# Performance work log

Hardware: AMD Instinct MI355X
Metric: run time of the kernel (lower is better)

The kernel has to match this reference:

```python
import jax, jax.numpy as jnp
import numpy as np

N_NODES = 100000
N_EDGES = 1600000
NFEAT, NHID, NCLASS = 128, 64, 16


def gcn_conv(x, W, edge_index, edge_weight, num_nodes):
    # PyG GCNConv (normalize=False, add_self_loops=False, bias=False):
    # h = x @ W ; out[i] = sum over edges (j->i) of edge_weight * h[j]
    h = x @ W                                  # [N, out]
    src, dst = edge_index[0], edge_index[1]
    msgs = h[src] * edge_weight[:, None]       # [E, out] gathered messages
    return jax.ops.segment_sum(msgs, dst, num_segments=num_nodes)


def setup_inputs() -> dict:
    key = jax.random.key(0)
    k = jax.random.split(key, 7)
    x = jax.random.normal(k[0], (N_NODES, NFEAT), dtype=jnp.float32)
    edge_index1 = jax.random.randint(k[1], (2, N_EDGES), 0, N_NODES, dtype=jnp.int32)
    edge_index2 = jax.random.randint(k[2], (2, N_EDGES), 0, N_NODES, dtype=jnp.int32)
    edge_weight1 = jax.random.uniform(k[3], (N_EDGES,), dtype=jnp.float32)
    edge_weight2 = jax.random.uniform(k[4], (N_EDGES,), dtype=jnp.float32)
    # Glorot-style linear weights (GCNConv lin, bias=False)
    W1 = jax.random.normal(k[5], (NFEAT, NHID), dtype=jnp.float32) / np.sqrt(NFEAT)
    W2 = jax.random.normal(k[6], (NHID, NCLASS), dtype=jnp.float32) / np.sqrt(NHID)
    return {"x": x, "edge_index1": edge_index1, "edge_index2": edge_index2,
            "edge_weight1": edge_weight1, "edge_weight2": edge_weight2,
            "W1": W1, "W2": W2}


def reference(x, edge_index1, edge_index2, edge_weight1, edge_weight2, W1, W2):
    n = x.shape[0]
    h = jax.nn.relu(gcn_conv(x, W1, edge_index1, edge_weight1, n))
    out = gcn_conv(h, W2, edge_index2, edge_weight2, n)
    return out
```

## Files before the change

kernel.cpp:

```cpp
#include <hip/hip_runtime.h>
#include <hip/hip_bf16.h>


#define EPB 4096
#define NBMAX 512
#define CAP 6144

__global__ __launch_bounds__(256) void gemm1_hist_kernel(
        const float* __restrict__ x, const float* __restrict__ W1,
        __hip_bfloat16* __restrict__ h1,
        const int* __restrict__ ei1, const int* __restrict__ ei2,
        int* __restrict__ hist_g, int n_nodes, int n_edges, int nblk, int nb,
        int gemm_blocks) {
    __shared__ float As[32][132];
    __shared__ float Bs[32][64];
    __shared__ int hist[NBMAX];
    int tid = threadIdx.x;

    if (blockIdx.x < gemm_blocks) {
        int node0 = blockIdx.x * 128;
        int n4 = (tid & 31) * 4;
        int f8 = (tid >> 5) * 8;
        float acc[4][8];
#pragma unroll
        for (int i = 0; i < 4; ++i)
#pragma unroll
            for (int j = 0; j < 8; ++j) acc[i][j] = 0.f;

        const float4* x4 = reinterpret_cast<const float4*>(x);
        const float4* W4 = reinterpret_cast<const float4*>(W1);

        for (int s = 0; s < 4; ++s) {
#pragma unroll
            for (int j = 0; j < 4; ++j) {
                int idx = tid + j * 256;
                int n = idx >> 3;
                int kq = idx & 7;
                float4 v = make_float4(0.f, 0.f, 0.f, 0.f);
                if (node0 + n < n_nodes) v = x4[(size_t)(node0 + n) * 32 + s * 8 + kq];
                int k4 = kq * 4;
                As[k4 + 0][n] = v.x;
                As[k4 + 1][n] = v.y;
                As[k4 + 2][n] = v.z;
                As[k4 + 3][n] = v.w;
            }
#pragma unroll
            for (int j = 0; j < 2; ++j) {
                int idx = tid + j * 256;
                int k = idx >> 4;
                int fq = idx & 15;
                *reinterpret_cast<float4*>(&Bs[k][fq * 4]) = W4[(size_t)(s * 32 + k) * 16 + fq];
            }
            __syncthreads();
#pragma unroll
            for (int kk = 0; kk < 32; ++kk) {
                float4 a = *reinterpret_cast<const float4*>(&As[kk][n4]);
                float4 b0 = *reinterpret_cast<const float4*>(&Bs[kk][f8]);
                float4 b1 = *reinterpret_cast<const float4*>(&Bs[kk][f8 + 4]);
                float av[4] = {a.x, a.y, a.z, a.w};
                float bv[8] = {b0.x, b0.y, b0.z, b0.w, b1.x, b1.y, b1.z, b1.w};
#pragma unroll
                for (int i = 0; i < 4; ++i)
#pragma unroll
                    for (int j = 0; j < 8; ++j) acc[i][j] += av[i] * bv[j];
            }
            __syncthreads();
        }
#pragma unroll
        for (int i = 0; i < 4; ++i) {
            int n = node0 + n4 + i;
            if (n < n_nodes) {
                __hip_bfloat16 tmp[8];
#pragma unroll
                for (int j = 0; j < 8; ++j) tmp[j] = __float2bfloat16(acc[i][j]);
                *reinterpret_cast<uint4*>(&h1[(size_t)n * 64 + f8]) =
                    *reinterpret_cast<const uint4*>(tmp);
            }
        }
    } else {
        int blk = blockIdx.x - gemm_blocks;
        int layer = (blk >= nblk) ? 1 : 0;
        int lblk = blk - layer * nblk;
        const int* ei = layer ? ei2 : ei1;
        for (int i = tid; i < nb; i += 256) hist[i] = 0;
        __syncthreads();
        int e0 = lblk * EPB;
#pragma unroll
        for (int j = 0; j < EPB / 256; ++j) {
            int e = e0 + tid + j * 256;
            if (e < n_edges) atomicAdd(&hist[ei[n_edges + e] >> 8], 1);
        }
        __syncthreads();
        int base = layer * nb * nblk;
        for (int i = tid; i < nb; i += 256) hist_g[base + i * nblk + lblk] = hist[i];
    }
}

__global__ void scan_local_k(int* __restrict__ data, int* __restrict__ bsums, int n) {
    __shared__ int tmp[1024];
    int i = blockIdx.x * 1024 + threadIdx.x;
    int v = (i < n) ? data[i] : 0;
    tmp[threadIdx.x] = v;
    __syncthreads();
    for (int off = 1; off < 1024; off <<= 1) {
        int t = (threadIdx.x >= off) ? tmp[threadIdx.x - off] : 0;
        __syncthreads();
        tmp[threadIdx.x] += t;
        __syncthreads();
    }
    if (i < n) data[i] = tmp[threadIdx.x] - v;
    if (threadIdx.x == 1023) bsums[blockIdx.x] = tmp[1023];
}

__global__ void bin_scatter_kernel(const int* __restrict__ ei1, const int* __restrict__ ei2,
                                   const float* __restrict__ ew1, const float* __restrict__ ew2,
                                   const int* __restrict__ scan_g, const int* __restrict__ bsums,
                                   int2* __restrict__ rec_out,
                                   int n_edges, int nblk, int nb, int nbk) {
    __shared__ int2 srec[EPB];
    __shared__ unsigned short sbkt[EPB];
    __shared__ int loff[NBMAX], cur[NBMAX], gbase[NBMAX];
    __shared__ int p[256];
    __shared__ int bscan[512];
    int tid = threadIdx.x, blk = blockIdx.x;
    int layer = (blk >= nblk) ? 1 : 0;
    int lblk = blk - layer * nblk;
    const int* ei = layer ? ei2 : ei1;
    const float* ew = layer ? ew2 : ew1;
    int n_scan_tot = 2 * nb * nblk;
    int total = 2 * n_edges;
    int base = layer * nb * nblk;
    int e0 = lblk * EPB;
    int cnt = min(EPB, n_edges - e0);

    {
        int t2 = tid * 2;
        int v0 = (t2 < nbk) ? bsums[t2] : 0;
        int v1 = (t2 + 1 < nbk) ? bsums[t2 + 1] : 0;
        p[tid] = v0 + v1;
        __syncthreads();
        for (int off = 1; off < 256; off <<= 1) {
            int t = (tid >= off) ? p[tid - off] : 0;
            __syncthreads();
            p[tid] += t;
            __syncthreads();
        }
        int pb = (tid > 0) ? p[tid - 1] : 0;
        bscan[t2] = pb;
        bscan[t2 + 1] = pb + v0;
        __syncthreads();
    }

    for (int i = tid; i < nb; i += 256) {
        int l = base + i * nblk + lblk;
        int g = scan_g[l] + bscan[l >> 10];
        int nxt = (l + 1 < n_scan_tot) ? (scan_g[l + 1] + bscan[(l + 1) >> 10]) : total;
        gbase[i] = g;
        loff[i] = nxt - g;
    }
    __syncthreads();
    int b0 = tid * 2;
    int c0 = (b0 < nb) ? loff[b0] : 0;
    int c1 = (b0 + 1 < nb) ? loff[b0 + 1] : 0;
    p[tid] = c0 + c1;
    __syncthreads();
    for (int off = 1; off < 256; off <<= 1) {
        int t = (tid >= off) ? p[tid - off] : 0;
        __syncthreads();
        p[tid] += t;
        __syncthreads();
    }
    int pbase = (tid > 0) ? p[tid - 1] : 0;
    __syncthreads();
    if (b0 < nb)     { loff[b0] = pbase;          cur[b0] = pbase; }
    if (b0 + 1 < nb) { loff[b0 + 1] = pbase + c0; cur[b0 + 1] = pbase + c0; }
    __syncthreads();
#pragma unroll
    for (int j = 0; j < EPB / 256; ++j) {
        int e = e0 + tid + j * 256;
        if (e < n_edges) {
            int s = ei[e], d = ei[n_edges + e];
            int b = d >> 8;
            int r = atomicAdd(&cur[b], 1);
            srec[r] = make_int2(s | ((d & 255) << 20), __float_as_int(ew[e]));
            sbkt[r] = (unsigned short)b;
        }
    }
    __syncthreads();
    for (int i = tid; i < cnt; i += 256) {
        int b = sbkt[i];
        rec_out[gbase[b] + (i - loff[b])] = srec[i];
    }
}


__global__ __launch_bounds__(256) void bucket_sort_kernel(
        const int2* __restrict__ rec_in, const int* __restrict__ scan_g,
        const int* __restrict__ bsums,
        int2* __restrict__ rec_out, int* __restrict__ rowptr1, int* __restrict__ rowptr2,
        int n_nodes, int n_edges, int nblk, int nb, int nbk) {
    __shared__ int2 srec[CAP];
    __shared__ int hist[256], cur[256], rp[256], p[256];
    __shared__ int bscan[512];
    int tid = threadIdx.x, b = blockIdx.x;
    int layer = (b >= nb) ? 1 : 0;
    int lb = b - layer * nb;
    int* rowptr = layer ? rowptr2 : rowptr1;
    int sh = layer ? 6 : 7;
    int total = 2 * n_edges;

    {
        int t2 = tid * 2;
        int v0 = (t2 < nbk) ? bsums[t2] : 0;
        int v1 = (t2 + 1 < nbk) ? bsums[t2 + 1] : 0;
        p[tid] = v0 + v1;
        __syncthreads();
        for (int off = 1; off < 256; off <<= 1) {
            int t = (tid >= off) ? p[tid - off] : 0;
            __syncthreads();
            p[tid] += t;
            __syncthreads();
        }
        int pb = (tid > 0) ? p[tid - 1] : 0;
        bscan[t2] = pb;
        bscan[t2 + 1] = pb + v0;
        __syncthreads();
    }

    int l0 = b * nblk;
    int start = scan_g[l0] + bscan[l0 >> 10];
    int l1 = (b + 1) * nblk;
    int end = (b + 1 < 2 * nb) ? (scan_g[l1] + bscan[l1 >> 10]) : total;
    int cnt = end - start;
    hist[tid] = 0;
    __syncthreads();
    for (int i = tid; i < cnt; i += 256) {
        int2 r = rec_in[start + i];
        atomicAdd(&hist[(r.x >> 20) & 255], 1);
    }
    __syncthreads();
    int v = hist[tid];
    rp[tid] = v;
    __syncthreads();
    for (int off = 1; off < 256; off <<= 1) {
        int t = (tid >= off) ? rp[tid - off] : 0;
        __syncthreads();
        rp[tid] += t;
        __syncthreads();
    }
    int excl = rp[tid] - v;
    cur[tid] = excl;
    int node = (lb << 8) + tid;
    if (node < n_nodes) rowptr[node] = start + excl;
    if (lb == nb - 1 && tid == 0) rowptr[n_nodes] = end;
    __syncthreads();
    for (int i = tid; i < cnt; i += 256) {
        int2 r = rec_in[start + i];
        int rk = atomicAdd(&cur[(r.x >> 20) & 255], 1);
        r.x = (r.x & 0xFFFFF) << sh;
        if (rk < CAP) srec[rk] = r;
    }
    __syncthreads();
    int lim = min(cnt, CAP);
    for (int i = tid; i < lim; i += 256) rec_out[start + i] = srec[i];
}


#define G1_EDGE(rr, aa) \
    aa += __bfloat162float(*(const __hip_bfloat16*)(h1b + (unsigned)(rr).x + f2)) * \
          __int_as_float((rr).y)

__global__ __launch_bounds__(256) void gather1_kernel(const __hip_bfloat16* __restrict__ h1,
                                                      const int* __restrict__ rowptr,
                                                      const int2* __restrict__ rec,
                                                      const float* __restrict__ W2,
                                                      float* __restrict__ h2, int n_nodes) {
    int tid = threadIdx.x;
    int w = tid >> 6, f = tid & 63;
    unsigned f2 = (unsigned)(f << 1);
    const char* h1b = (const char*)h1;
    int n = blockIdx.x * 4 + w;
    bool valid = (n < n_nodes);
    int i = 0, end = 0;
    if (valid) { i = rowptr[n]; end = rowptr[n + 1]; }
    float a0 = 0.f, a1 = 0.f, a2 = 0.f, a3 = 0.f;
    float a4 = 0.f, a5 = 0.f, a6 = 0.f, a7 = 0.f;
    float a8 = 0.f, a9 = 0.f, a10 = 0.f, a11 = 0.f;
    float a12 = 0.f, a13 = 0.f, a14 = 0.f, a15 = 0.f;
    for (; i + 15 < end; i += 16) {
        int2 r0 = rec[i],      r1 = rec[i + 1],  r2 = rec[i + 2],  r3 = rec[i + 3];
        int2 r4 = rec[i + 4],  r5 = rec[i + 5],  r6 = rec[i + 6],  r7 = rec[i + 7];
        int2 r8 = rec[i + 8],  r9 = rec[i + 9],  r10 = rec[i + 10], r11 = rec[i + 11];
        int2 r12 = rec[i + 12], r13 = rec[i + 13], r14 = rec[i + 14], r15 = rec[i + 15];
        G1_EDGE(r0, a0);   G1_EDGE(r1, a1);   G1_EDGE(r2, a2);   G1_EDGE(r3, a3);
        G1_EDGE(r4, a4);   G1_EDGE(r5, a5);   G1_EDGE(r6, a6);   G1_EDGE(r7, a7);
        G1_EDGE(r8, a8);   G1_EDGE(r9, a9);   G1_EDGE(r10, a10); G1_EDGE(r11, a11);
        G1_EDGE(r12, a12); G1_EDGE(r13, a13); G1_EDGE(r14, a14); G1_EDGE(r15, a15);
    }
    for (; i + 7 < end; i += 8) {
        int2 r0 = rec[i],     r1 = rec[i + 1], r2 = rec[i + 2], r3 = rec[i + 3];
        int2 r4 = rec[i + 4], r5 = rec[i + 5], r6 = rec[i + 6], r7 = rec[i + 7];
        G1_EDGE(r0, a0); G1_EDGE(r1, a1); G1_EDGE(r2, a2); G1_EDGE(r3, a3);
        G1_EDGE(r4, a4); G1_EDGE(r5, a5); G1_EDGE(r6, a6); G1_EDGE(r7, a7);
    }
    for (; i + 3 < end; i += 4) {
        int2 r0 = rec[i], r1 = rec[i + 1], r2 = rec[i + 2], r3 = rec[i + 3];
        G1_EDGE(r0, a0); G1_EDGE(r1, a1); G1_EDGE(r2, a2); G1_EDGE(r3, a3);
    }
    for (; i < end; ++i) {
        int2 r = rec[i];
        G1_EDGE(r, a0);
    }
    float s0 = ((a0 + a1) + (a2 + a3)) + ((a4 + a5) + (a6 + a7));
    float s1 = ((a8 + a9) + (a10 + a11)) + ((a12 + a13) + (a14 + a15));
    float r = fmaxf(s0 + s1, 0.f);
    int c = f & 15, kq = f >> 4;
    float pacc = 0.f;
#pragma unroll
    for (int j = 0; j < 16; ++j) {
        int k = kq * 16 + j;
        float rk = __shfl(r, k, 64);
        pacc += rk * W2[k * 16 + c];
    }
    pacc += __shfl_xor(pacc, 16, 64);
    pacc += __shfl_xor(pacc, 32, 64);
    if (valid && f < 16) h2[(size_t)n * 16 + f] = pacc;
}


#define G2_EDGE(rr, aa) \
    aa += *(const float*)(h2b + (unsigned)(rr).x + f4) * __int_as_float((rr).y)

__global__ void gather2_kernel(const float* __restrict__ h2,
                               const int* __restrict__ rowptr,
                               const int2* __restrict__ rec,
                               float* __restrict__ out, int n_nodes) {
    int n = blockIdx.x * 16 + (threadIdx.x >> 4);
    if (n >= n_nodes) return;
    int f = threadIdx.x & 15;
    unsigned f4 = (unsigned)(f << 2);
    const char* h2b = (const char*)h2;
    int i = rowptr[n], end = rowptr[n + 1];
    float a0 = 0.f, a1 = 0.f, a2 = 0.f, a3 = 0.f;
    float a4 = 0.f, a5 = 0.f, a6 = 0.f, a7 = 0.f;
    for (; i + 7 < end; i += 8) {
        int2 r0 = rec[i],     r1 = rec[i + 1], r2 = rec[i + 2], r3 = rec[i + 3];
        int2 r4 = rec[i + 4], r5 = rec[i + 5], r6 = rec[i + 6], r7 = rec[i + 7];
        G2_EDGE(r0, a0); G2_EDGE(r1, a1); G2_EDGE(r2, a2); G2_EDGE(r3, a3);
        G2_EDGE(r4, a4); G2_EDGE(r5, a5); G2_EDGE(r6, a6); G2_EDGE(r7, a7);
    }
    for (; i + 3 < end; i += 4) {
        int2 r0 = rec[i], r1 = rec[i + 1], r2 = rec[i + 2], r3 = rec[i + 3];
        G2_EDGE(r0, a0); G2_EDGE(r1, a1); G2_EDGE(r2, a2); G2_EDGE(r3, a3);
    }
    for (; i < end; ++i) {
        int2 r = rec[i];
        G2_EDGE(r, a0);
    }
    out[(size_t)n * 16 + f] = (((a0 + a1) + (a2 + a3)) + ((a4 + a5) + (a6 + a7)));
}


extern "C" void kernel_launch(void* const* d_in, const int* in_sizes, int n_in,
                              void* d_out, int out_size, void* d_ws, size_t ws_size,
                              hipStream_t stream) {
    const float* x   = (const float*)d_in[0];
    const int*   ei1 = (const int*)d_in[1];
    const int*   ei2 = (const int*)d_in[2];
    const float* ew1 = (const float*)d_in[3];
    const float* ew2 = (const float*)d_in[4];
    const float* W1  = (const float*)d_in[5];
    const float* W2  = (const float*)d_in[6];

    const int n_nodes = in_sizes[0] / 128;
    const int n_edges = in_sizes[1] / 2;
    const int nb   = (n_nodes + 255) >> 8;
    const int nblk = (n_edges + EPB - 1) / EPB;
    const int n_scan_tot = 2 * nb * nblk;
    const int scan_blocks = (n_scan_tot + 1023) / 1024;
    const int gemm_blocks = (n_nodes + 127) / 128;

    int2* rec2   = (int2*)d_ws;
    int2* recbuf = rec2 + (size_t)2 * n_edges;
    int*  hist_g = (int*)(recbuf + (size_t)2 * n_edges);
    int*  bsums  = hist_g + n_scan_tot;
    int*  rowptr1 = bsums + 512;
    int*  rowptr2 = rowptr1 + n_nodes + 1;
    __hip_bfloat16* h1 = (__hip_bfloat16*)(rowptr2 + n_nodes + 1);
    float* h2 = (float*)recbuf;
    float* out = (float*)d_out;

    gemm1_hist_kernel<<<gemm_blocks + 2 * nblk, 256, 0, stream>>>(
        x, W1, h1, ei1, ei2, hist_g, n_nodes, n_edges, nblk, nb, gemm_blocks);
    scan_local_k<<<scan_blocks, 1024, 0, stream>>>(hist_g, bsums, n_scan_tot);
    bin_scatter_kernel<<<2 * nblk, 256, 0, stream>>>(ei1, ei2, ew1, ew2, hist_g, bsums,
                                                     recbuf, n_edges, nblk, nb, scan_blocks);
    bucket_sort_kernel<<<2 * nb, 256, 0, stream>>>(recbuf, hist_g, bsums, rec2,
                                                   rowptr1, rowptr2,
                                                   n_nodes, n_edges, nblk, nb, scan_blocks);

    gather1_kernel<<<(n_nodes + 3) / 4, 256, 0, stream>>>(h1, rowptr1, rec2, W2, h2, n_nodes);
    gather2_kernel<<<(n_nodes + 15) / 16, 256, 0, stream>>>(h2, rowptr2, rec2, out, n_nodes);
}
```

Before: 300.4 us.

## Split bucket sort per layer and overlap layer-2 sort with layer-1 gather

The single bucket sort kernel is split in two. The layer-1 sort runs alone, and the layer-2 sort now runs in the same launch as the layer-1 gather/GEMM, as extra blocks. The shared-memory staging buffer is also removed, so sorted records are scattered straight to global memory. The aim is to fill the GPU during the small layer-2 sort and cut LDS use so more blocks fit per CU. The cost is less coalesced record writes, and h2 must not overlap the layer-2 source records that are read concurrently.

```diff
diff --git a/kernel.cpp b/kernel.cpp
--- a/kernel.cpp
+++ b/kernel.cpp
@@ -4,7 +4,6 @@
 
 #define EPB 4096
 #define NBMAX 512
-#define CAP 6144
 
 __global__ __launch_bounds__(256) void gemm1_hist_kernel(
         const float* __restrict__ x, const float* __restrict__ W1,
@@ -194,20 +193,14 @@
 }
 
 
-__global__ __launch_bounds__(256) void bucket_sort_kernel(
+__global__ __launch_bounds__(256) void bucket_sort_l1_kernel(
         const int2* __restrict__ rec_in, const int* __restrict__ scan_g,
         const int* __restrict__ bsums,
-        int2* __restrict__ rec_out, int* __restrict__ rowptr1, int* __restrict__ rowptr2,
+        int2* __restrict__ rec_out, int* __restrict__ rowptr1,
         int n_nodes, int n_edges, int nblk, int nb, int nbk) {
-    __shared__ int2 srec[CAP];
     __shared__ int hist[256], cur[256], rp[256], p[256];
     __shared__ int bscan[512];
     int tid = threadIdx.x, b = blockIdx.x;
-    int layer = (b >= nb) ? 1 : 0;
-    int lb = b - layer * nb;
-    int* rowptr = layer ? rowptr2 : rowptr1;
-    int sh = layer ? 6 : 7;
-    int total = 2 * n_edges;
 
     {
         int t2 = tid * 2;
@@ -230,7 +223,7 @@
     int l0 = b * nblk;
     int start = scan_g[l0] + bscan[l0 >> 10];
     int l1 = (b + 1) * nblk;
-    int end = (b + 1 < 2 * nb) ? (scan_g[l1] + bscan[l1 >> 10]) : total;
+    int end = scan_g[l1] + bscan[l1 >> 10];
     int cnt = end - start;
     hist[tid] = 0;
     __syncthreads();
@@ -250,19 +243,16 @@
     }
     int excl = rp[tid] - v;
     cur[tid] = excl;
-    int node = (lb << 8) + tid;
-    if (node < n_nodes) rowptr[node] = start + excl;
-    if (lb == nb - 1 && tid == 0) rowptr[n_nodes] = end;
+    int node = (b << 8) + tid;
+    if (node < n_nodes) rowptr1[node] = start + excl;
+    if (b == nb - 1 && tid == 0) rowptr1[n_nodes] = end;
     __syncthreads();
     for (int i = tid; i < cnt; i += 256) {
         int2 r = rec_in[start + i];
         int rk = atomicAdd(&cur[(r.x >> 20) & 255], 1);
-        r.x = (r.x & 0xFFFFF) << sh;
-        if (rk < CAP) srec[rk] = r;
-    }
-    __syncthreads();
-    int lim = min(cnt, CAP);
-    for (int i = tid; i < lim; i += 256) rec_out[start + i] = srec[i];
+        r.x = (r.x & 0xFFFFF) << 7;
+        rec_out[start + rk] = r;
+    }
 }
 
 
@@ -270,61 +260,125 @@
     aa += __bfloat162float(*(const __hip_bfloat16*)(h1b + (unsigned)(rr).x + f2)) * \
           __int_as_float((rr).y)
 
-__global__ __launch_bounds__(256) void gather1_kernel(const __hip_bfloat16* __restrict__ h1,
-                                                      const int* __restrict__ rowptr,
-                                                      const int2* __restrict__ rec,
-                                                      const float* __restrict__ W2,
-                                                      float* __restrict__ h2, int n_nodes) {
+__global__ __launch_bounds__(256) void sortl2_gather1_kernel(
+        const int2* __restrict__ rec_in, const int* __restrict__ scan_g,
+        const int* __restrict__ bsums, int2* __restrict__ rec2,
+        int* __restrict__ rowptr2,
+        const __hip_bfloat16* __restrict__ h1, const int* __restrict__ rowptr1,
+        const float* __restrict__ W2, float* __restrict__ h2,
+        int n_nodes, int n_edges, int nblk, int nb, int nbk) {
+    __shared__ int hist[256], cur[256], rp[256], p[256];
+    __shared__ int bscan[512];
     int tid = threadIdx.x;
-    int w = tid >> 6, f = tid & 63;
-    unsigned f2 = (unsigned)(f << 1);
-    const char* h1b = (const char*)h1;
-    int n = blockIdx.x * 4 + w;
-    bool valid = (n < n_nodes);
-    int i = 0, end = 0;
-    if (valid) { i = rowptr[n]; end = rowptr[n + 1]; }
-    float a0 = 0.f, a1 = 0.f, a2 = 0.f, a3 = 0.f;
-    float a4 = 0.f, a5 = 0.f, a6 = 0.f, a7 = 0.f;
-    float a8 = 0.f, a9 = 0.f, a10 = 0.f, a11 = 0.f;
-    float a12 = 0.f, a13 = 0.f, a14 = 0.f, a15 = 0.f;
-    for (; i + 15 < end; i += 16) {
-        int2 r0 = rec[i],      r1 = rec[i + 1],  r2 = rec[i + 2],  r3 = rec[i + 3];
-        int2 r4 = rec[i + 4],  r5 = rec[i + 5],  r6 = rec[i + 6],  r7 = rec[i + 7];
-        int2 r8 = rec[i + 8],  r9 = rec[i + 9],  r10 = rec[i + 10], r11 = rec[i + 11];
-        int2 r12 = rec[i + 12], r13 = rec[i + 13], r14 = rec[i + 14], r15 = rec[i + 15];
-        G1_EDGE(r0, a0);   G1_EDGE(r1, a1);   G1_EDGE(r2, a2);   G1_EDGE(r3, a3);
-        G1_EDGE(r4, a4);   G1_EDGE(r5, a5);   G1_EDGE(r6, a6);   G1_EDGE(r7, a7);
-        G1_EDGE(r8, a8);   G1_EDGE(r9, a9);   G1_EDGE(r10, a10); G1_EDGE(r11, a11);
-        G1_EDGE(r12, a12); G1_EDGE(r13, a13); G1_EDGE(r14, a14); G1_EDGE(r15, a15);
-    }
-    for (; i + 7 < end; i += 8) {
-        int2 r0 = rec[i],     r1 = rec[i + 1], r2 = rec[i + 2], r3 = rec[i + 3];
-        int2 r4 = rec[i + 4], r5 = rec[i + 5], r6 = rec[i + 6], r7 = rec[i + 7];
-        G1_EDGE(r0, a0); G1_EDGE(r1, a1); G1_EDGE(r2, a2); G1_EDGE(r3, a3);
-        G1_EDGE(r4, a4); G1_EDGE(r5, a5); G1_EDGE(r6, a6); G1_EDGE(r7, a7);
-    }
-    for (; i + 3 < end; i += 4) {
-        int2 r0 = rec[i], r1 = rec[i + 1], r2 = rec[i + 2], r3 = rec[i + 3];
-        G1_EDGE(r0, a0); G1_EDGE(r1, a1); G1_EDGE(r2, a2); G1_EDGE(r3, a3);
-    }
-    for (; i < end; ++i) {
-        int2 r = rec[i];
-        G1_EDGE(r, a0);
-    }
-    float s0 = ((a0 + a1) + (a2 + a3)) + ((a4 + a5) + (a6 + a7));
-    float s1 = ((a8 + a9) + (a10 + a11)) + ((a12 + a13) + (a14 + a15));
-    float r = fmaxf(s0 + s1, 0.f);
-    int c = f & 15, kq = f >> 4;
-    float pacc = 0.f;
-#pragma unroll
-    for (int j = 0; j < 16; ++j) {
-        int k = kq * 16 + j;
-        float rk = __shfl(r, k, 64);
-        pacc += rk * W2[k * 16 + c];
-    }
-    pacc += __shfl_xor(pacc, 16, 64);
-    pacc += __shfl_xor(pacc, 32, 64);
-    if (valid && f < 16) h2[(size_t)n * 16 + f] = pacc;
+
+    if (blockIdx.x < nb) {
+        int lb = blockIdx.x;
+        int b2 = nb + lb;
+        int total = 2 * n_edges;
+
+        {
+            int t2 = tid * 2;
+            int v0 = (t2 < nbk) ? bsums[t2] : 0;
+            int v1 = (t2 + 1 < nbk) ? bsums[t2 + 1] : 0;
+            p[tid] = v0 + v1;
+            __syncthreads();
+            for (int off = 1; off < 256; off <<= 1) {
+                int t = (tid >= off) ? p[tid - off] : 0;
+                __syncthreads();
+                p[tid] += t;
+                __syncthreads();
+            }
+            int pb = (tid > 0) ? p[tid - 1] : 0;
+            bscan[t2] = pb;
+            bscan[t2 + 1] = pb + v0;
+            __syncthreads();
+        }
+
+        int l0 = b2 * nblk;
+        int start = scan_g[l0] + bscan[l0 >> 10];
+        int l1 = (b2 + 1) * nblk;
+        int end = (b2 + 1 < 2 * nb) ? (scan_g[l1] + bscan[l1 >> 10]) : total;
+        int cnt = end - start;
+        hist[tid] = 0;
+        __syncthreads();
+        for (int i = tid; i < cnt; i += 256) {
+            int2 r = rec_in[start + i];
+            atomicAdd(&hist[(r.x >> 20) & 255], 1);
+        }
+        __syncthreads();
+        int v = hist[tid];
+        rp[tid] = v;
+        __syncthreads();
+        for (int off = 1; off < 256; off <<= 1) {
+            int t = (tid >= off) ? rp[tid - off] : 0;
+            __syncthreads();
+            rp[tid] += t;
+            __syncthreads();
+        }
+        int excl = rp[tid] - v;
+        cur[tid] = excl;
+        int node = (lb << 8) + tid;
+        if (node < n_nodes) rowptr2[node] = start + excl;
+        if (lb == nb - 1 && tid == 0) rowptr2[n_nodes] = end;
+        __syncthreads();
+        for (int i = tid; i < cnt; i += 256) {
+            int2 r = rec_in[start + i];
+            int rk = atomicAdd(&cur[(r.x >> 20) & 255], 1);
+            r.x = (r.x & 0xFFFFF) << 6;
+            rec2[start + rk] = r;
+        }
+    } else {
+        int w = tid >> 6, f = tid & 63;
+        unsigned f2 = (unsigned)(f << 1);
+        const char* h1b = (const char*)h1;
+        int n = (blockIdx.x - nb) * 4 + w;
+        bool valid = (n < n_nodes);
+        int i = 0, end = 0;
+        if (valid) { i = rowptr1[n]; end = rowptr1[n + 1]; }
+        float a0 = 0.f, a1 = 0.f, a2 = 0.f, a3 = 0.f;
+        float a4 = 0.f, a5 = 0.f, a6 = 0.f, a7 = 0.f;
+        float a8 = 0.f, a9 = 0.f, a10 = 0.f, a11 = 0.f;
+        float a12 = 0.f, a13 = 0.f, a14 = 0.f, a15 = 0.f;
+        const int2* rec = rec2;
+        for (; i + 15 < end; i += 16) {
+            int2 r0 = rec[i],      r1 = rec[i + 1],  r2 = rec[i + 2],  r3 = rec[i + 3];
+            int2 r4 = rec[i + 4],  r5 = rec[i + 5],  r6 = rec[i + 6],  r7 = rec[i + 7];
+            int2 r8 = rec[i + 8],  r9 = rec[i + 9],  r10 = rec[i + 10], r11 = rec[i + 11];
+            int2 r12 = rec[i + 12], r13 = rec[i + 13], r14 = rec[i + 14], r15 = rec[i + 15];
+            G1_EDGE(r0, a0);   G1_EDGE(r1, a1);   G1_EDGE(r2, a2);   G1_EDGE(r3, a3);
+            G1_EDGE(r4, a4);   G1_EDGE(r5, a5);   G1_EDGE(r6, a6);   G1_EDGE(r7, a7);
+            G1_EDGE(r8, a8);   G1_EDGE(r9, a9);   G1_EDGE(r10, a10); G1_EDGE(r11, a11);
+            G1_EDGE(r12, a12); G1_EDGE(r13, a13); G1_EDGE(r14, a14); G1_EDGE(r15, a15);
+        }
+        for (; i + 7 < end; i += 8) {
+            int2 r0 = rec[i],     r1 = rec[i + 1], r2 = rec[i + 2], r3 = rec[i + 3];
+            int2 r4 = rec[i + 4], r5 = rec[i + 5], r6 = rec[i + 6], r7 = rec[i + 7];
+            G1_EDGE(r0, a0); G1_EDGE(r1, a1); G1_EDGE(r2, a2); G1_EDGE(r3, a3);
+            G1_EDGE(r4, a4); G1_EDGE(r5, a5); G1_EDGE(r6, a6); G1_EDGE(r7, a7);
+        }
+        for (; i + 3 < end; i += 4) {
+            int2 r0 = rec[i], r1 = rec[i + 1], r2 = rec[i + 2], r3 = rec[i + 3];
+            G1_EDGE(r0, a0); G1_EDGE(r1, a1); G1_EDGE(r2, a2); G1_EDGE(r3, a3);
+        }
+        for (; i < end; ++i) {
+            int2 r = rec[i];
+            G1_EDGE(r, a0);
+        }
+        float s0 = ((a0 + a1) + (a2 + a3)) + ((a4 + a5) + (a6 + a7));
+        float s1 = ((a8 + a9) + (a10 + a11)) + ((a12 + a13) + (a14 + a15));
+        float r = fmaxf(s0 + s1, 0.f);
+        int c = f & 15, kq = f >> 4;
+        float pacc = 0.f;
+#pragma unroll
+        for (int j = 0; j < 16; ++j) {
+            int k = kq * 16 + j;
+            float rk = __shfl(r, k, 64);
+            pacc += rk * W2[k * 16 + c];
+        }
+        pacc += __shfl_xor(pacc, 16, 64);
+        pacc += __shfl_xor(pacc, 32, 64);
+        if (valid && f < 16) h2[(size_t)n * 16 + f] = pacc;
+    }
 }
 
 
@@ -379,6 +433,7 @@
     const int n_scan_tot = 2 * nb * nblk;
     const int scan_blocks = (n_scan_tot + 1023) / 1024;
     const int gemm_blocks = (n_nodes + 127) / 128;
+    const int g1_blocks = (n_nodes + 3) / 4;
 
     int2* rec2   = (int2*)d_ws;
     int2* recbuf = rec2 + (size_t)2 * n_edges;
@@ -395,10 +450,10 @@
     scan_local_k<<<scan_blocks, 1024, 0, stream>>>(hist_g, bsums, n_scan_tot);
     bin_scatter_kernel<<<2 * nblk, 256, 0, stream>>>(ei1, ei2, ew1, ew2, hist_g, bsums,
                                                      recbuf, n_edges, nblk, nb, scan_blocks);
-    bucket_sort_kernel<<<2 * nb, 256, 0, stream>>>(recbuf, hist_g, bsums, rec2,
-                                                   rowptr1, rowptr2,
-                                                   n_nodes, n_edges, nblk, nb, scan_blocks);
-
-    gather1_kernel<<<(n_nodes + 3) / 4, 256, 0, stream>>>(h1, rowptr1, rec2, W2, h2, n_nodes);
+    bucket_sort_l1_kernel<<<nb, 256, 0, stream>>>(recbuf, hist_g, bsums, rec2, rowptr1,
+                                                  n_nodes, n_edges, nblk, nb, scan_blocks);
+    sortl2_gather1_kernel<<<nb + g1_blocks, 256, 0, stream>>>(
+        recbuf, hist_g, bsums, rec2, rowptr2, h1, rowptr1, W2, h2,
+        n_nodes, n_edges, nblk, nb, scan_blocks);
     gather2_kernel<<<(n_nodes + 15) / 16, 256, 0, stream>>>(h2, rowptr2, rec2, out, n_nodes);
 }
```

Measured after the change: 301.0 us. Within noise of the previous version (+0.2%).
